# Optimization experiments

Hardware: AMD Instinct MI355X
Metric: run time of the kernel (lower is better)

The kernel has to match this reference:

```python
import jax, jax.numpy as jnp
import numpy as np

N = 16384      # number of nodes (pos rows)
S = 16384      # number of src nodes (src_pos rows)
E = 262144     # number of edges (COO entries)
D = 512        # embed_dim
H = 8          # num_heads
HD = D // H    # head_dim = 64
HID = 1024     # mlp hidden
MLP_IN = D + 3 * H  # 536
EPS = 1e-5


def layer_norm(x, g, b):
    mu = jnp.mean(x, axis=-1, keepdims=True)
    var = jnp.mean((x - mu) ** 2, axis=-1, keepdims=True)
    return (x - mu) * jax.lax.rsqrt(var + EPS) * g + b


def setup_inputs() -> dict:
    key = jax.random.key(0)
    ks = jax.random.split(key, 20)
    s = 1.0 / np.sqrt(D)
    sh = 1.0 / np.sqrt(HID)
    return {
        "x": jax.random.normal(ks[0], (N, D), jnp.float32),
        "Wq": jax.random.uniform(ks[1], (D, D), jnp.float32, -s, s),
        "bq": jnp.zeros((D,), jnp.float32),
        "Wk": jax.random.uniform(ks[2], (D, D), jnp.float32, -s, s),
        "bk": jnp.zeros((D,), jnp.float32),
        "g_att": jnp.ones((D,), jnp.float32),
        "b_att": jnp.zeros((D,), jnp.float32),
        "g_mlp": jnp.ones((D,), jnp.float32),
        "b_mlp": jnp.zeros((D,), jnp.float32),
        "W_in": jax.random.uniform(ks[3], (HID, MLP_IN), jnp.float32, -s, s),
        "b_in": jnp.zeros((HID,), jnp.float32),
        "W_out": jax.random.uniform(ks[4], (D, HID), jnp.float32, -sh, sh),
        "b_out": jnp.zeros((D,), jnp.float32),
        "att_bias": jax.random.normal(ks[5], (H, E), jnp.float32),
        "dist": jax.random.uniform(ks[6], (E,), jnp.float32, 0.5, 6.0),
        "pos": jax.random.normal(ks[7], (N, 3), jnp.float32),
        "src_pos": jax.random.normal(ks[8], (S, 3), jnp.float32),
        "row_index": jax.random.randint(ks[9], (E,), 0, N),
        "src_index": jax.random.randint(ks[10], (E,), 0, S),
        "org_to_src": jax.random.randint(ks[11], (S,), 0, N),
    }


def reference(x, Wq, bq, Wk, bk, g_att, b_att, g_mlp, b_mlp, W_in, b_in,
              W_out, b_out, att_bias, dist, pos, src_pos,
              row_index, src_index, org_to_src):
    n = x.shape[0]
    z = layer_norm(x, g_att, b_att)
    q = (z @ Wq.T + bq).reshape(n, H, HD)          # [N,H,hd]
    k = (z @ Wk.T + bk).reshape(n, H, HD)          # [N,H,hd]
    k_src = k[org_to_src]                          # [S,H,hd]
    # per-edge masked logits: q[row] . k_src[col] / sqrt(hd) + bias
    qe = q[row_index]                              # [E,H,hd]
    ke = k_src[src_index]                          # [E,H,hd]
    logits = jnp.einsum('ehd,ehd->eh', qe, ke) / jnp.sqrt(jnp.float32(HD))
    logits = logits + att_bias.T                   # [E,H]
    # segment (per-row) softmax over incident edges
    m = jax.ops.segment_max(logits, row_index, num_segments=n)
    p = jnp.exp(logits - m[row_index])
    den = jax.ops.segment_sum(p, row_index, num_segments=n)
    att = p / den[row_index]                       # [E,H]
    inv = jnp.where(dist == 0, 0.0, 1.0 / dist)[:, None]
    att = att * inv
    # sparse bmm: feat[h,row] += att * src_pos[col]; rowsum for centering
    sp = src_pos[src_index]                        # [E,3]
    feat = jax.ops.segment_sum(att[:, :, None] * sp[:, None, :],
                               row_index, num_segments=n)   # [N,H,3]
    rowsum = jax.ops.segment_sum(att, row_index, num_segments=n)  # [N,H]
    feat = feat - rowsum[:, :, None] * pos[:, None, :]
    feat = feat.reshape(n, H * 3)
    z2 = layer_norm(x, g_mlp, b_mlp)
    h = jax.nn.gelu(jnp.concatenate([z2, feat], axis=-1) @ W_in.T + b_in)
    return x + (h @ W_out.T + b_out)
```

## Files before the change

### kernel.cpp

```cpp
#include <hip/hip_runtime.h>
#include <math.h>


typedef unsigned short u16;
typedef __attribute__((ext_vector_type(8))) short bf16x8;
typedef __attribute__((ext_vector_type(4))) float f32x4;
typedef __attribute__((ext_vector_type(2))) float f32x2;

constexpr int N_NODES = 16384;
constexpr int E_EDGES = 262144;
constexpr int D = 512;
constexpr int KIN = 576;

constexpr size_t OFF_ZATT = 0;
constexpr size_t OFF_ZCAT = 16777216;
constexpr size_t OFF_WQK  = 35651584;
constexpr size_t OFF_BQK  = 36700160;
constexpr size_t OFF_WIN  = 36704256;
constexpr size_t OFF_WOUT = 37883904;
constexpr size_t OFF_QK   = 38932480;
constexpr size_t OFF_CNT  = 55709696;
constexpr size_t OFF_BKT  = 55775232;
constexpr size_t OFF_HBF  = 59969536;

static __device__ __forceinline__ u16 f2bf(float f) {
  union { float f; unsigned int u; } v; v.f = f;
  unsigned int u = v.u;
  u = u + 0x7FFFu + ((u >> 16) & 1u);
  return (u16)(u >> 16);
}
static __device__ __forceinline__ void gload16(const u16* g, u16* l) {
  __builtin_amdgcn_global_load_lds(
      (const __attribute__((address_space(1))) unsigned int*)g,
      (__attribute__((address_space(3))) unsigned int*)l, 16, 0, 0);
}

__global__ __launch_bounds__(256) void prep_weights(
    const float* __restrict__ Wq, const float* __restrict__ Wk,
    const float* __restrict__ bq, const float* __restrict__ bk,
    const float* __restrict__ W_in, const float* __restrict__ W_out,
    const int* __restrict__ row_index,
    const float* __restrict__ att_bias, const float* __restrict__ dist,
    const float* __restrict__ src_pos, const int* __restrict__ src_index,
    const int* __restrict__ org_to_src,
    u16* __restrict__ wqk, float* __restrict__ bqk,
    u16* __restrict__ win, u16* __restrict__ wout,
    int* __restrict__ cnt, int* __restrict__ bucket, float* __restrict__ rec)
{
  const int gid = blockIdx.x * 256 + threadIdx.x;
  if (gid < 512 * 1024) {
    wqk[gid]  = f2bf(gid < 512 * 512 ? Wq[gid] : Wk[gid - 512 * 512]);
    wout[gid] = f2bf(W_out[gid]);
  }
  if (gid < 1024 * KIN) {
    const int r = gid / KIN, c = gid - r * KIN;
    win[gid] = f2bf(c < 536 ? W_in[r * 536 + c] : 0.f);
  }
  if (gid < 1024) bqk[gid] = gid < 512 ? bq[gid] : bk[gid - 512];
  if (gid < E_EDGES) {
    const int r = row_index[gid];
    const int p = atomicAdd(&cnt[r], 1);
    if (p < 64) bucket[(size_t)r * 64 + p] = gid;
    const int s = src_index[gid];
    const float dv = dist[gid];
    float4 q0, q1, q2, q3;
    q0.x = att_bias[gid];
    q0.y = att_bias[(size_t)1 * E_EDGES + gid];
    q0.z = att_bias[(size_t)2 * E_EDGES + gid];
    q0.w = att_bias[(size_t)3 * E_EDGES + gid];
    q1.x = att_bias[(size_t)4 * E_EDGES + gid];
    q1.y = att_bias[(size_t)5 * E_EDGES + gid];
    q1.z = att_bias[(size_t)6 * E_EDGES + gid];
    q1.w = att_bias[(size_t)7 * E_EDGES + gid];
    q2.x = (dv == 0.f) ? 0.f : 1.f / dv;
    q2.y = src_pos[(size_t)s * 3 + 0];
    q2.z = src_pos[(size_t)s * 3 + 1];
    q2.w = src_pos[(size_t)s * 3 + 2];
    q3.x = __int_as_float(org_to_src[s]);
    q3.y = 0.f; q3.z = 0.f; q3.w = 0.f;
    float4* rg = (float4*)(rec + (size_t)gid * 16);
    rg[0] = q0; rg[1] = q1; rg[2] = q2; rg[3] = q3;
  }
}

__global__ __launch_bounds__(256) void ln_kernel(
    const float* __restrict__ x,
    const float* __restrict__ g1, const float* __restrict__ b1,
    const float* __restrict__ g2, const float* __restrict__ b2,
    u16* __restrict__ zatt, u16* __restrict__ zcat)
{
  const int row = blockIdx.x;
  const int t = threadIdx.x;
  const float2 v = *(const float2*)(x + (size_t)row * D + t * 2);
  float s = v.x + v.y;
  float s2 = v.x * v.x + v.y * v.y;
#pragma unroll
  for (int m = 1; m < 64; m <<= 1) {
    s  += __shfl_xor(s, m, 64);
    s2 += __shfl_xor(s2, m, 64);
  }
  __shared__ float red[8];
  const int wv = t >> 6;
  if ((t & 63) == 0) { red[wv] = s; red[4 + wv] = s2; }
  __syncthreads();
  s  = red[0] + red[1] + red[2] + red[3];
  s2 = red[4] + red[5] + red[6] + red[7];
  const float mu = s * (1.f / D);
  const float var = s2 * (1.f / D) - mu * mu;
  const float rs = rsqrtf(var + 1e-5f);
  const int c0 = t * 2;
  const float n0 = (v.x - mu) * rs, n1 = (v.y - mu) * rs;
  zatt[(size_t)row * D + c0]       = f2bf(n0 * g1[c0] + b1[c0]);
  zatt[(size_t)row * D + c0 + 1]   = f2bf(n1 * g1[c0 + 1] + b1[c0 + 1]);
  zcat[(size_t)row * KIN + c0]     = f2bf(n0 * g2[c0] + b2[c0]);
  zcat[(size_t)row * KIN + c0 + 1] = f2bf(n1 * g2[c0 + 1] + b2[c0 + 1]);
  if (t < 64) zcat[(size_t)row * KIN + D + t] = 0;
}


#define MM_BLK(AF, BF, NB) do {                                               \
  __builtin_amdgcn_s_setprio(1);                                              \
  _Pragma("unroll")                                                           \
  for (int mi = 0; mi < 8; ++mi) {                                            \
    acc[mi][NB]     = __builtin_amdgcn_mfma_f32_16x16x32_bf16(AF[mi], BF[0], acc[mi][NB], 0, 0, 0);     \
    acc[mi][NB + 1] = __builtin_amdgcn_mfma_f32_16x16x32_bf16(AF[mi], BF[1], acc[mi][NB + 1], 0, 0, 0); \
  }                                                                           \
  __builtin_amdgcn_s_setprio(0);                                              \
} while (0)

template <int EPI>
__global__ __launch_bounds__(512, 2) void gemm256(
    const u16* __restrict__ A, const u16* __restrict__ B,
    const float* __restrict__ bias,
    void* __restrict__ Cout, int M, int Nn, int K)
{
  extern __shared__ __align__(16) u16 lds[];
  const int tid = threadIdx.x;
  const int lane = tid & 63;
  const int wave = tid >> 6;
  const int wave_m = wave >> 2;
  const int wave_n = wave & 3;
  const int m0 = blockIdx.x * 256;
  const int n0 = blockIdx.y * 256;
  const int fr = lane & 15;
  const int fq = lane >> 4;
  const int NT = K >> 6;

  f32x4 acc[8][4];
#pragma unroll
  for (int i = 0; i < 8; ++i)
#pragma unroll
    for (int j = 0; j < 4; ++j) acc[i][j] = 0.f;

  auto stageA = [&](int slot, int ktile, int kh) {
    u16* base = lds + slot * 8192;
    const int kb = ktile * 64 + kh * 32;
#pragma unroll
    for (int r = 0; r < 2; ++r) {
      const int g = r * 512 + tid;
      gload16(A + (size_t)(m0 + (g >> 2)) * K + kb + (g & 3) * 8,
              base + (r * 512 + wave * 64) * 8);
    }
  };
  auto stageB = [&](int slot, int ktile, int kh) {
    u16* base = lds + 32768 + slot * 8192;
    const int kb = ktile * 64 + kh * 32;
#pragma unroll
    for (int r = 0; r < 2; ++r) {
      const int g = r * 512 + tid;
      gload16(B + (size_t)(n0 + (g >> 2)) * K + kb + (g & 3) * 8,
              base + (r * 512 + wave * 64) * 8);
    }
  };
  auto ldA = [&](bf16x8 (&af)[8], int slot) {
    const u16* p = lds + slot * 8192 + (wave_m * 128 + fr) * 32 + fq * 8;
#pragma unroll
    for (int mi = 0; mi < 8; ++mi)
      af[mi] = *(const bf16x8*)(p + mi * 16 * 32);
  };
  auto ldB = [&](bf16x8 (&bf)[2], int slot, int nh) {
    const u16* p = lds + 32768 + slot * 8192 + (wave_n * 64 + nh * 32 + fr) * 32 + fq * 8;
    bf[0] = *(const bf16x8*)(p);
    bf[1] = *(const bf16x8*)(p + 16 * 32);
  };

  stageA(0, 0, 0); stageB(0, 0, 0);
  stageA(1, 0, 1); stageB(1, 0, 1);
  stageA(2, 1, 0); stageB(2, 1, 0);
  stageA(3, 1, 1);
  asm volatile("s_waitcnt vmcnt(10)" ::: "memory");
  __builtin_amdgcn_s_barrier();
  asm volatile("" ::: "memory");

  bf16x8 af[8], bf0[2], bf1[2];
  for (int t = 0; t < NT; ++t) {
    const int sa0 = (2 * t) & 3,  sa1 = (2 * t + 1) & 3;
    const int sb1n = (2 * t + 3) & 3;
    const int t1 = (t + 1 >= NT) ? t + 1 - NT : t + 1;
    const int t2 = (t + 2 >= NT) ? t + 2 - NT : t + 2;

    ldA(af, sa0); ldB(bf0, sa0, 0);
    stageB(sb1n, t1, 1);
    __builtin_amdgcn_s_barrier();
    asm volatile("" ::: "memory");
    MM_BLK(af, bf0, 0);
    __builtin_amdgcn_s_barrier();
    asm volatile("" ::: "memory");
    ldB(bf1, sa0, 1);
    stageA(sa0, t2, 0);
    __builtin_amdgcn_s_barrier();
    asm volatile("" ::: "memory");
    MM_BLK(af, bf1, 2);
    asm volatile("s_waitcnt vmcnt(10)" ::: "memory");
    __builtin_amdgcn_s_barrier();
    asm volatile("" ::: "memory");
    ldA(af, sa1); ldB(bf0, sa1, 0);
    stageB(sa0, t2, 0);
    __builtin_amdgcn_s_barrier();
    asm volatile("" ::: "memory");
    MM_BLK(af, bf0, 0);
    __builtin_amdgcn_s_barrier();
    asm volatile("" ::: "memory");
    ldB(bf1, sa1, 1);
    stageA(sa1, t2, 1);
    __builtin_amdgcn_s_barrier();
    asm volatile("" ::: "memory");
    MM_BLK(af, bf1, 2);
    asm volatile("s_waitcnt vmcnt(10)" ::: "memory");
    __builtin_amdgcn_s_barrier();
    asm volatile("" ::: "memory");
  }
  asm volatile("s_waitcnt vmcnt(0)" ::: "memory");

#pragma unroll
  for (int mi = 0; mi < 8; ++mi) {
#pragma unroll
    for (int nj = 0; nj < 4; ++nj) {
      const int col = n0 + wave_n * 64 + nj * 16 + fr;
      const float bv = bias[col];
#pragma unroll
      for (int rr = 0; rr < 4; ++rr) {
        const int row = m0 + wave_m * 128 + mi * 16 + fq * 4 + rr;
        float v = acc[mi][nj][rr] + bv;
        if (EPI == 1) {
          const float nu = -1.5957691216057308f * (v + 0.044715f * v * v * v);
          const float sg = __builtin_amdgcn_rcpf(1.f + __expf(nu));
          ((u16*)Cout)[(size_t)row * Nn + col] = f2bf(v * sg);
        } else {
          const int pk = __builtin_amdgcn_cvt_pk_fp8_f32(v, v, 0, false);
          ((unsigned char*)Cout)[(size_t)row * Nn + col] = (unsigned char)(pk & 0xFF);
        }
      }
    }
  }
}

template <int EPI, int WPE>
__global__ __launch_bounds__(256, WPE) void gemm_nt(
    const u16* __restrict__ A, const u16* __restrict__ B,
    const float* __restrict__ bias, const float* __restrict__ resid,
    void* __restrict__ Cout, int M, int Nn, int K)
{
  constexpr int BM = 128, BN = 128, BK = 32;
  __shared__ __align__(16) u16 As[2 * BM * BK];
  __shared__ __align__(16) u16 Bs[2 * BN * BK];
  const int tid = threadIdx.x;
  const int lane = tid & 63;
  const int wave = tid >> 6;
  const int m0 = blockIdx.x * BM;
  const int n0 = blockIdx.y * BN;
  const int wm = (wave >> 1) * 64;
  const int wn = (wave & 1) * 64;
  const int fr = lane & 15;
  const int fq = lane >> 4;
  const int srow = lane >> 2;
  const int skoff = (lane & 3) * 8;

  f32x4 acc[4][4];
#pragma unroll
  for (int i = 0; i < 4; ++i)
#pragma unroll
    for (int j = 0; j < 4; ++j) acc[i][j] = 0.f;

  for (int k0 = 0; k0 < K; k0 += 2 * BK) {
    __syncthreads();
#pragma unroll
    for (int t = 0; t < 2; ++t) {
#pragma unroll
      for (int r = 0; r < 2; ++r) {
        const int rowbase = r * 64 + wave * 16;
        gload16(A + (size_t)(m0 + rowbase + srow) * K + k0 + t * BK + skoff,
                As + t * (BM * BK) + rowbase * BK);
        gload16(B + (size_t)(n0 + rowbase + srow) * K + k0 + t * BK + skoff,
                Bs + t * (BN * BK) + rowbase * BK);
      }
    }
    __syncthreads();
#pragma unroll
    for (int t = 0; t < 2; ++t) {
      bf16x8 af[4], bfr[4];
#pragma unroll
      for (int mi = 0; mi < 4; ++mi)
        af[mi] = *(const bf16x8*)(As + t * (BM * BK) + (wm + mi * 16 + fr) * BK + fq * 8);
#pragma unroll
      for (int ni = 0; ni < 4; ++ni)
        bfr[ni] = *(const bf16x8*)(Bs + t * (BN * BK) + (wn + ni * 16 + fr) * BK + fq * 8);
#pragma unroll
      for (int mi = 0; mi < 4; ++mi)
#pragma unroll
        for (int ni = 0; ni < 4; ++ni)
          acc[mi][ni] = __builtin_amdgcn_mfma_f32_16x16x32_bf16(af[mi], bfr[ni], acc[mi][ni], 0, 0, 0);
    }
  }

#pragma unroll
  for (int mi = 0; mi < 4; ++mi) {
#pragma unroll
    for (int ni = 0; ni < 4; ++ni) {
      const int col = n0 + wn + ni * 16 + fr;
      const float bv = bias[col];
#pragma unroll
      for (int rr = 0; rr < 4; ++rr) {
        const int row = m0 + wm + mi * 16 + fq * 4 + rr;
        float v = acc[mi][ni][rr] + bv;
        if (EPI == 1) {
          const float nu = -1.5957691216057308f * (v + 0.044715f * v * v * v);
          const float sg = __builtin_amdgcn_rcpf(1.f + __expf(nu));
          ((u16*)Cout)[(size_t)row * Nn + col] = f2bf(v * sg);
        } else if (EPI == 2) {
          ((float*)Cout)[(size_t)row * Nn + col] = v + resid[(size_t)row * Nn + col];
        } else {
          const int pk = __builtin_amdgcn_cvt_pk_fp8_f32(v, v, 0, false);
          ((unsigned char*)Cout)[(size_t)row * Nn + col] = (unsigned char)(pk & 0xFF);
        }
      }
    }
  }
}

__global__ __launch_bounds__(256) void edge_csr(
    const unsigned char* __restrict__ qk8, const float* __restrict__ rec,
    const int* __restrict__ cnt, const int* __restrict__ bucket,
    const float* __restrict__ pos, u16* __restrict__ zcat)
{
  const int lane = threadIdx.x & 63;
  const int wave = threadIdx.x >> 6;
  const int row = blockIdx.x * 4 + wave;
  const int half = lane >> 5;
  const int sub = lane & 31;
  const int h = sub >> 2, j = sub & 3;
  const int deg = min(cnt[row], 64);
  const int base = row * 64;

  const uint4 qv = *(const uint4*)(qk8 + (size_t)row * 1024 + sub * 16);
  float qf[16];
  {
    const unsigned int* qu = (const unsigned int*)&qv;
#pragma unroll
    for (int i = 0; i < 4; ++i) {
      const f32x2 lo = __builtin_amdgcn_cvt_pk_f32_fp8(qu[i], false);
      const f32x2 hi = __builtin_amdgcn_cvt_pk_f32_fp8(qu[i], true);
      qf[i * 4 + 0] = lo.x; qf[i * 4 + 1] = lo.y;
      qf[i * 4 + 2] = hi.x; qf[i * 4 + 3] = hi.y;
    }
  }

  float accA = 0.f, accB = 0.f;
  const int npair = (deg + 1) >> 1;

  bool ok0 = half < deg;
  int e0 = ok0 ? bucket[base + half] : 0;
  const float* r0 = rec + (size_t)e0 * 16;
  float bias0 = r0[h];
  float invd0 = r0[8];
  float spA0 = (j >= 2) ? r0[7 + j] : 0.f;
  float spB0 = (j == 1) ? r0[11] : 0.f;
  uint4 kv0 = *(const uint4*)(qk8 + (size_t)__float_as_int(r0[12]) * 1024 + 512 + sub * 16);

  bool ok1 = 2 + half < deg;
  int e1 = ok1 ? bucket[base + 2 + half] : 0;
  const float* r1 = rec + (size_t)e1 * 16;
  float bias1 = r1[h];
  float invd1 = r1[8];
  float spA1 = (j >= 2) ? r1[7 + j] : 0.f;
  float spB1 = (j == 1) ? r1[11] : 0.f;
  int kr1 = __float_as_int(r1[12]);

  bool ok2 = 4 + half < deg;
  int e2 = ok2 ? bucket[base + 4 + half] : 0;

  for (int i = 0; i < npair; ++i) {
    const uint4 kv1 = *(const uint4*)(qk8 + (size_t)kr1 * 1024 + 512 + sub * 16);
    const float* r2 = rec + (size_t)e2 * 16;
    const float bias2 = r2[h];
    const float invd2 = r2[8];
    const float spA2 = (j >= 2) ? r2[7 + j] : 0.f;
    const float spB2 = (j == 1) ? r2[11] : 0.f;
    const int kr2 = __float_as_int(r2[12]);
    const bool ok3 = 2 * (i + 3) + half < deg;
    const int e3 = ok3 ? bucket[base + 2 * (i + 3) + half] : 0;

    float p;
    {
      const unsigned int* ku = (const unsigned int*)&kv0;
      const f32x2 a0 = __builtin_amdgcn_cvt_pk_f32_fp8(ku[0], false);
      const f32x2 a1 = __builtin_amdgcn_cvt_pk_f32_fp8(ku[0], true);
      const f32x2 b0 = __builtin_amdgcn_cvt_pk_f32_fp8(ku[1], false);
      const f32x2 b1 = __builtin_amdgcn_cvt_pk_f32_fp8(ku[1], true);
      const f32x2 c0 = __builtin_amdgcn_cvt_pk_f32_fp8(ku[2], false);
      const f32x2 c1 = __builtin_amdgcn_cvt_pk_f32_fp8(ku[2], true);
      const f32x2 d0 = __builtin_amdgcn_cvt_pk_f32_fp8(ku[3], false);
      const f32x2 d1 = __builtin_amdgcn_cvt_pk_f32_fp8(ku[3], true);
      p = qf[0] * a0.x;
      p = fmaf(qf[1],  a0.y, p);  p = fmaf(qf[2],  a1.x, p);  p = fmaf(qf[3],  a1.y, p);
      p = fmaf(qf[4],  b0.x, p);  p = fmaf(qf[5],  b0.y, p);  p = fmaf(qf[6],  b1.x, p);
      p = fmaf(qf[7],  b1.y, p);  p = fmaf(qf[8],  c0.x, p);  p = fmaf(qf[9],  c0.y, p);
      p = fmaf(qf[10], c1.x, p);  p = fmaf(qf[11], c1.y, p);  p = fmaf(qf[12], d0.x, p);
      p = fmaf(qf[13], d0.y, p);  p = fmaf(qf[14], d1.x, p);  p = fmaf(qf[15], d1.y, p);
    }
    p += __shfl_xor(p, 1, 64);
    p += __shfl_xor(p, 2, 64);
    float pe = __expf(p * 0.125f + bias0);
    pe = ok0 ? pe : 0.f;
    const float w = pe * invd0;
    accA += (j == 0) ? pe : (j == 1) ? w : w * spA0;
    accB += w * spB0;

    ok0 = ok1; bias0 = bias1; invd0 = invd1; spA0 = spA1; spB0 = spB1; kv0 = kv1;
    ok1 = ok2; bias1 = bias2; invd1 = invd2; spA1 = spA2; spB1 = spB2; kr1 = kr2;
    ok2 = ok3; e2 = e3;
  }

  accA += __shfl_xor(accA, 32, 64);
  accB += __shfl_xor(accB, 32, 64);
  const int hb = h << 2;
  const float den  = __shfl(accA, hb + 0, 64);
  const float wsum = __shfl(accA, hb + 1, 64);
  const float wsp01 = __shfl(accA, hb + 2 + (j & 1), 64);
  const float wsp2  = __shfl(accB, hb + 1, 64);
  const float invd = (den != 0.f) ? 1.f / den : 0.f;
  const float rsum = wsum * invd;
  if (half == 0 && j < 3) {
    const float wspj = (j < 2) ? wsp01 : wsp2;
    zcat[(size_t)row * KIN + D + h * 3 + j] = f2bf(wspj * invd - rsum * pos[row * 3 + j]);
  }
}

extern "C" void kernel_launch(void* const* d_in, const int* in_sizes, int n_in,
                              void* d_out, int out_size, void* d_ws, size_t ws_size,
                              hipStream_t stream)
{
  const float* x        = (const float*)d_in[0];
  const float* Wq       = (const float*)d_in[1];
  const float* bq       = (const float*)d_in[2];
  const float* Wk       = (const float*)d_in[3];
  const float* bk       = (const float*)d_in[4];
  const float* g_att    = (const float*)d_in[5];
  const float* b_att    = (const float*)d_in[6];
  const float* g_mlp    = (const float*)d_in[7];
  const float* b_mlp    = (const float*)d_in[8];
  const float* W_in     = (const float*)d_in[9];
  const float* b_in     = (const float*)d_in[10];
  const float* W_out    = (const float*)d_in[11];
  const float* b_out    = (const float*)d_in[12];
  const float* att_bias = (const float*)d_in[13];
  const float* dist     = (const float*)d_in[14];
  const float* pos      = (const float*)d_in[15];
  const float* src_pos  = (const float*)d_in[16];
  const int* row_index  = (const int*)d_in[17];
  const int* src_index  = (const int*)d_in[18];
  const int* org_to_src = (const int*)d_in[19];

  char* ws = (char*)d_ws;
  u16*   zatt = (u16*)(ws + OFF_ZATT);
  u16*   zcat = (u16*)(ws + OFF_ZCAT);
  u16*   wqk  = (u16*)(ws + OFF_WQK);
  float* bqk  = (float*)(ws + OFF_BQK);
  u16*   win  = (u16*)(ws + OFF_WIN);
  u16*   wout = (u16*)(ws + OFF_WOUT);
  unsigned char* qk8 = (unsigned char*)(ws + OFF_QK);
  int*   cnt  = (int*)(ws + OFF_CNT);
  int*   bkt  = (int*)(ws + OFF_BKT);
  u16*   hbf  = (u16*)(ws + OFF_HBF);
  float* rec  = (float*)(ws + OFF_HBF);

  static bool s_attr = false;
  if (!s_attr) {
    hipFuncSetAttribute(reinterpret_cast<const void*>(&gemm256<4>),
                        hipFuncAttributeMaxDynamicSharedMemorySize, 131072);
    hipFuncSetAttribute(reinterpret_cast<const void*>(&gemm256<1>),
                        hipFuncAttributeMaxDynamicSharedMemorySize, 131072);
    s_attr = true;
  }

  hipMemsetAsync(ws + OFF_CNT, 0, 65536, stream);

  prep_weights<<<2304, 256, 0, stream>>>(Wq, Wk, bq, bk, W_in, W_out, row_index,
                                         att_bias, dist, src_pos, src_index, org_to_src,
                                         wqk, bqk, win, wout, cnt, bkt, rec);
  ln_kernel<<<N_NODES, 256, 0, stream>>>(x, g_att, b_att, g_mlp, b_mlp, zatt, zcat);
  gemm256<4><<<dim3(64, 4), 512, 131072, stream>>>(zatt, wqk, bqk, qk8, N_NODES, 1024, 512);
  edge_csr<<<N_NODES / 4, 256, 0, stream>>>(qk8, rec, cnt, bkt, pos, zcat);
  gemm256<1><<<dim3(64, 4), 512, 131072, stream>>>(zcat, win, b_in, hbf, N_NODES, 1024, KIN);
  gemm_nt<2, 2><<<dim3(128, 4), 256, 0, stream>>>(hbf, wout, b_out, x, d_out, N_NODES, 512, 1024);
}
```

Baseline: 263.2 us.

## Merge prep and layernorm kernels, swizzle GEMM LDS, deepen edge prefetch

```diff
diff --git a/kernel.cpp b/kernel.cpp
--- a/kernel.cpp
+++ b/kernel.cpp
@@ -35,7 +35,7 @@
       (__attribute__((address_space(3))) unsigned int*)l, 16, 0, 0);
 }
 
-__global__ __launch_bounds__(256) void prep_weights(
+__global__ __launch_bounds__(256) void prep_ln(
     const float* __restrict__ Wq, const float* __restrict__ Wk,
     const float* __restrict__ bq, const float* __restrict__ bk,
     const float* __restrict__ W_in, const float* __restrict__ W_out,
@@ -45,51 +45,51 @@
     const int* __restrict__ org_to_src,
     u16* __restrict__ wqk, float* __restrict__ bqk,
     u16* __restrict__ win, u16* __restrict__ wout,
-    int* __restrict__ cnt, int* __restrict__ bucket, float* __restrict__ rec)
-{
-  const int gid = blockIdx.x * 256 + threadIdx.x;
-  if (gid < 512 * 1024) {
-    wqk[gid]  = f2bf(gid < 512 * 512 ? Wq[gid] : Wk[gid - 512 * 512]);
-    wout[gid] = f2bf(W_out[gid]);
-  }
-  if (gid < 1024 * KIN) {
-    const int r = gid / KIN, c = gid - r * KIN;
-    win[gid] = f2bf(c < 536 ? W_in[r * 536 + c] : 0.f);
-  }
-  if (gid < 1024) bqk[gid] = gid < 512 ? bq[gid] : bk[gid - 512];
-  if (gid < E_EDGES) {
-    const int r = row_index[gid];
-    const int p = atomicAdd(&cnt[r], 1);
-    if (p < 64) bucket[(size_t)r * 64 + p] = gid;
-    const int s = src_index[gid];
-    const float dv = dist[gid];
-    float4 q0, q1, q2, q3;
-    q0.x = att_bias[gid];
-    q0.y = att_bias[(size_t)1 * E_EDGES + gid];
-    q0.z = att_bias[(size_t)2 * E_EDGES + gid];
-    q0.w = att_bias[(size_t)3 * E_EDGES + gid];
-    q1.x = att_bias[(size_t)4 * E_EDGES + gid];
-    q1.y = att_bias[(size_t)5 * E_EDGES + gid];
-    q1.z = att_bias[(size_t)6 * E_EDGES + gid];
-    q1.w = att_bias[(size_t)7 * E_EDGES + gid];
-    q2.x = (dv == 0.f) ? 0.f : 1.f / dv;
-    q2.y = src_pos[(size_t)s * 3 + 0];
-    q2.z = src_pos[(size_t)s * 3 + 1];
-    q2.w = src_pos[(size_t)s * 3 + 2];
-    q3.x = __int_as_float(org_to_src[s]);
-    q3.y = 0.f; q3.z = 0.f; q3.w = 0.f;
-    float4* rg = (float4*)(rec + (size_t)gid * 16);
-    rg[0] = q0; rg[1] = q1; rg[2] = q2; rg[3] = q3;
-  }
-}
-
-__global__ __launch_bounds__(256) void ln_kernel(
+    int* __restrict__ cnt, int* __restrict__ bucket, float* __restrict__ rec,
     const float* __restrict__ x,
     const float* __restrict__ g1, const float* __restrict__ b1,
     const float* __restrict__ g2, const float* __restrict__ b2,
     u16* __restrict__ zatt, u16* __restrict__ zcat)
 {
-  const int row = blockIdx.x;
+  __shared__ float red[8];
+  if (blockIdx.x < 2304) {
+    const int gid = blockIdx.x * 256 + threadIdx.x;
+    if (gid < 512 * 1024) {
+      wqk[gid]  = f2bf(gid < 512 * 512 ? Wq[gid] : Wk[gid - 512 * 512]);
+      wout[gid] = f2bf(W_out[gid]);
+    }
+    if (gid < 1024 * KIN) {
+      const int r = gid / KIN, c = gid - r * KIN;
+      win[gid] = f2bf(c < 536 ? W_in[r * 536 + c] : 0.f);
+    }
+    if (gid < 1024) bqk[gid] = gid < 512 ? bq[gid] : bk[gid - 512];
+    if (gid < E_EDGES) {
+      const int r = row_index[gid];
+      const int p = atomicAdd(&cnt[r], 1);
+      if (p < 64) bucket[(size_t)r * 64 + p] = gid;
+      const int s = src_index[gid];
+      const float dv = dist[gid];
+      float4 q0, q1, q2, q3;
+      q0.x = att_bias[gid];
+      q0.y = att_bias[(size_t)1 * E_EDGES + gid];
+      q0.z = att_bias[(size_t)2 * E_EDGES + gid];
+      q0.w = att_bias[(size_t)3 * E_EDGES + gid];
+      q1.x = att_bias[(size_t)4 * E_EDGES + gid];
+      q1.y = att_bias[(size_t)5 * E_EDGES + gid];
+      q1.z = att_bias[(size_t)6 * E_EDGES + gid];
+      q1.w = att_bias[(size_t)7 * E_EDGES + gid];
+      q2.x = (dv == 0.f) ? 0.f : 1.f / dv;
+      q2.y = src_pos[(size_t)s * 3 + 0];
+      q2.z = src_pos[(size_t)s * 3 + 1];
+      q2.w = src_pos[(size_t)s * 3 + 2];
+      q3.x = __int_as_float(org_to_src[s]);
+      q3.y = 0.f; q3.z = 0.f; q3.w = 0.f;
+      float4* rg = (float4*)(rec + (size_t)gid * 16);
+      rg[0] = q0; rg[1] = q1; rg[2] = q2; rg[3] = q3;
+    }
+    return;
+  }
+  const int row = blockIdx.x - 2304;
   const int t = threadIdx.x;
   const float2 v = *(const float2*)(x + (size_t)row * D + t * 2);
   float s = v.x + v.y;
@@ -99,7 +99,6 @@
     s  += __shfl_xor(s, m, 64);
     s2 += __shfl_xor(s2, m, 64);
   }
-  __shared__ float red[8];
   const int wv = t >> 6;
   if ((t & 63) == 0) { red[wv] = s; red[4 + wv] = s2; }
   __syncthreads();
@@ -145,6 +144,7 @@
   const int fr = lane & 15;
   const int fq = lane >> 4;
   const int NT = K >> 6;
+  const int sw = (fq ^ ((fr >> 1) & 3)) * 8;
 
   f32x4 acc[8][4];
 #pragma unroll
@@ -158,7 +158,9 @@
 #pragma unroll
     for (int r = 0; r < 2; ++r) {
       const int g = r * 512 + tid;
-      gload16(A + (size_t)(m0 + (g >> 2)) * K + kb + (g & 3) * 8,
+      const int row = g >> 2;
+      const int gs = (g & 3) ^ ((row >> 1) & 3);
+      gload16(A + (size_t)(m0 + row) * K + kb + gs * 8,
               base + (r * 512 + wave * 64) * 8);
     }
   };
@@ -168,18 +170,20 @@
 #pragma unroll
     for (int r = 0; r < 2; ++r) {
       const int g = r * 512 + tid;
-      gload16(B + (size_t)(n0 + (g >> 2)) * K + kb + (g & 3) * 8,
+      const int row = g >> 2;
+      const int gs = (g & 3) ^ ((row >> 1) & 3);
+      gload16(B + (size_t)(n0 + row) * K + kb + gs * 8,
               base + (r * 512 + wave * 64) * 8);
     }
   };
   auto ldA = [&](bf16x8 (&af)[8], int slot) {
-    const u16* p = lds + slot * 8192 + (wave_m * 128 + fr) * 32 + fq * 8;
+    const u16* p = lds + slot * 8192 + (wave_m * 128 + fr) * 32 + sw;
 #pragma unroll
     for (int mi = 0; mi < 8; ++mi)
       af[mi] = *(const bf16x8*)(p + mi * 16 * 32);
   };
   auto ldB = [&](bf16x8 (&bf)[2], int slot, int nh) {
-    const u16* p = lds + 32768 + slot * 8192 + (wave_n * 64 + nh * 32 + fr) * 32 + fq * 8;
+    const u16* p = lds + 32768 + slot * 8192 + (wave_n * 64 + nh * 32 + fr) * 32 + sw;
     bf[0] = *(const bf16x8*)(p);
     bf[1] = *(const bf16x8*)(p + 16 * 32);
   };
@@ -274,7 +278,8 @@
   const int fr = lane & 15;
   const int fq = lane >> 4;
   const int srow = lane >> 2;
-  const int skoff = (lane & 3) * 8;
+  const int skoff = ((lane & 3) ^ ((srow >> 1) & 3)) * 8;
+  const int sw = (fq ^ ((fr >> 1) & 3)) * 8;
 
   f32x4 acc[4][4];
 #pragma unroll
@@ -301,10 +306,10 @@
       bf16x8 af[4], bfr[4];
 #pragma unroll
       for (int mi = 0; mi < 4; ++mi)
-        af[mi] = *(const bf16x8*)(As + t * (BM * BK) + (wm + mi * 16 + fr) * BK + fq * 8);
+        af[mi] = *(const bf16x8*)(As + t * (BM * BK) + (wm + mi * 16 + fr) * BK + sw);
 #pragma unroll
       for (int ni = 0; ni < 4; ++ni)
-        bfr[ni] = *(const bf16x8*)(Bs + t * (BN * BK) + (wn + ni * 16 + fr) * BK + fq * 8);
+        bfr[ni] = *(const bf16x8*)(Bs + t * (BM * BK) + (wn + ni * 16 + fr) * BK + sw);
 #pragma unroll
       for (int mi = 0; mi < 4; ++mi)
 #pragma unroll
@@ -371,8 +376,7 @@
   bool ok0 = half < deg;
   int e0 = ok0 ? bucket[base + half] : 0;
   const float* r0 = rec + (size_t)e0 * 16;
-  float bias0 = r0[h];
-  float invd0 = r0[8];
+  float bias0 = r0[h], invd0 = r0[8];
   float spA0 = (j >= 2) ? r0[7 + j] : 0.f;
   float spB0 = (j == 1) ? r0[11] : 0.f;
   uint4 kv0 = *(const uint4*)(qk8 + (size_t)__float_as_int(r0[12]) * 1024 + 512 + sub * 16);
@@ -380,25 +384,31 @@
   bool ok1 = 2 + half < deg;
   int e1 = ok1 ? bucket[base + 2 + half] : 0;
   const float* r1 = rec + (size_t)e1 * 16;
-  float bias1 = r1[h];
-  float invd1 = r1[8];
+  float bias1 = r1[h], invd1 = r1[8];
   float spA1 = (j >= 2) ? r1[7 + j] : 0.f;
   float spB1 = (j == 1) ? r1[11] : 0.f;
-  int kr1 = __float_as_int(r1[12]);
+  uint4 kv1 = *(const uint4*)(qk8 + (size_t)__float_as_int(r1[12]) * 1024 + 512 + sub * 16);
 
   bool ok2 = 4 + half < deg;
   int e2 = ok2 ? bucket[base + 4 + half] : 0;
+  const float* r2p = rec + (size_t)e2 * 16;
+  float bias2 = r2p[h], invd2 = r2p[8];
+  float spA2 = (j >= 2) ? r2p[7 + j] : 0.f;
+  float spB2 = (j == 1) ? r2p[11] : 0.f;
+  int kr2 = __float_as_int(r2p[12]);
+
+  bool ok3 = 6 + half < deg;
+  int e3 = ok3 ? bucket[base + 6 + half] : 0;
 
   for (int i = 0; i < npair; ++i) {
-    const uint4 kv1 = *(const uint4*)(qk8 + (size_t)kr1 * 1024 + 512 + sub * 16);
-    const float* r2 = rec + (size_t)e2 * 16;
-    const float bias2 = r2[h];
-    const float invd2 = r2[8];
-    const float spA2 = (j >= 2) ? r2[7 + j] : 0.f;
-    const float spB2 = (j == 1) ? r2[11] : 0.f;
-    const int kr2 = __float_as_int(r2[12]);
-    const bool ok3 = 2 * (i + 3) + half < deg;
-    const int e3 = ok3 ? bucket[base + 2 * (i + 3) + half] : 0;
+    const uint4 kv2 = *(const uint4*)(qk8 + (size_t)kr2 * 1024 + 512 + sub * 16);
+    const float* r3 = rec + (size_t)e3 * 16;
+    const float bias3 = r3[h], invd3 = r3[8];
+    const float spA3 = (j >= 2) ? r3[7 + j] : 0.f;
+    const float spB3 = (j == 1) ? r3[11] : 0.f;
+    const int kr3 = __float_as_int(r3[12]);
+    const bool ok4 = 2 * (i + 4) + half < deg;
+    const int e4 = ok4 ? bucket[base + 2 * (i + 4) + half] : 0;
 
     float p;
     {
@@ -427,8 +437,9 @@
     accB += w * spB0;
 
     ok0 = ok1; bias0 = bias1; invd0 = invd1; spA0 = spA1; spB0 = spB1; kv0 = kv1;
-    ok1 = ok2; bias1 = bias2; invd1 = invd2; spA1 = spA2; spB1 = spB2; kr1 = kr2;
-    ok2 = ok3; e2 = e3;
+    ok1 = ok2; bias1 = bias2; invd1 = invd2; spA1 = spA2; spB1 = spB2; kv1 = kv2;
+    ok2 = ok3; bias2 = bias3; invd2 = invd3; spA2 = spA3; spB2 = spB3; kr2 = kr3;
+    ok3 = ok4; e3 = e4;
   }
 
   accA += __shfl_xor(accA, 32, 64);
@@ -495,10 +506,11 @@
 
   hipMemsetAsync(ws + OFF_CNT, 0, 65536, stream);
 
-  prep_weights<<<2304, 256, 0, stream>>>(Wq, Wk, bq, bk, W_in, W_out, row_index,
-                                         att_bias, dist, src_pos, src_index, org_to_src,
-                                         wqk, bqk, win, wout, cnt, bkt, rec);
-  ln_kernel<<<N_NODES, 256, 0, stream>>>(x, g_att, b_att, g_mlp, b_mlp, zatt, zcat);
+  prep_ln<<<2304 + N_NODES, 256, 0, stream>>>(
+      Wq, Wk, bq, bk, W_in, W_out, row_index,
+      att_bias, dist, src_pos, src_index, org_to_src,
+      wqk, bqk, win, wout, cnt, bkt, rec,
+      x, g_att, b_att, g_mlp, b_mlp, zatt, zcat);
   gemm256<4><<<dim3(64, 4), 512, 131072, stream>>>(zatt, wqk, bqk, qk8, N_NODES, 1024, 512);
   edge_csr<<<N_NODES / 4, 256, 0, stream>>>(qk8, rec, cnt, bkt, pos, zcat);
   gemm256<1><<<dim3(64, 4), 512, 131072, stream>>>(zcat, win, b_in, hbf, N_NODES, 1024, KIN);
```

Measured after the change: 258.1 us. 2.0% less time.
